# Kernel optimization log

Hardware: AMD Instinct MI355X
Metric: run time of the kernel (lower is better)

The kernel has to match this reference:

```python
import jax, jax.numpy as jnp
import numpy as np
import math

L, D, H, HD, F, G, V, P = 15, 512, 64, 8, 2048, 128, 7, 49
B, N = 4, 256


def setup_inputs() -> dict:
    key = jax.random.key(0)
    ks = jax.random.split(key, 24)
    nrm = lambda k, shape, s=0.02: (jax.random.normal(k, shape) * s).astype(jnp.float32)
    inp = {}
    inp["atom_types"] = jax.random.randint(ks[0], (B, N), 0, V)
    inp["coords"] = jax.random.normal(ks[1], (B, N, 3)) * 3.0
    inp["pair_types"] = jax.random.randint(ks[2], (B, N, N), 0, P)
    inp["mask"] = jnp.ones((B, N), dtype=bool)
    # embeddings / pair encoding params
    inp["atom_emb"] = nrm(ks[3], (V, D), 1.0).at[0].set(0.0)  # padding_idx=0
    inp["gaussian_mu"] = jax.random.normal(ks[4], (G,))
    inp["gaussian_sigma"] = jnp.ones((G,)) * 0.1
    inp["pair_a"] = jax.random.normal(ks[5], (P,)) * 0.01
    inp["pair_b"] = jax.random.normal(ks[6], (P,)) * 0.01
    inp["pl_w"] = nrm(ks[7], (G,))
    inp["pl_b"] = jnp.zeros(())
    # stacked per-layer params (leading dim L for lax.scan)
    inp["ln1_g"] = jnp.ones((L, D)); inp["ln1_b"] = jnp.zeros((L, D))
    inp["qkv_w"] = nrm(ks[8], (L, 3 * D, D)); inp["qkv_b"] = jnp.zeros((L, 3 * D))
    inp["pp_w"] = nrm(ks[9], (L, H), 0.1); inp["pp_b"] = jnp.zeros((L, H))
    inp["out_w"] = nrm(ks[10], (L, D, D)); inp["out_b"] = jnp.zeros((L, D))
    inp["ln2_g"] = jnp.ones((L, D)); inp["ln2_b"] = jnp.zeros((L, D))
    inp["ffn_w1"] = nrm(ks[11], (L, F, D)); inp["ffn_b1"] = jnp.zeros((L, F))
    inp["ffn_w2"] = nrm(ks[12], (L, D, F)); inp["ffn_b2"] = jnp.zeros((L, D))
    # SE3 head scalar affines (Linear(1,1) twice) and energy head
    inp["se3_uw"] = jnp.array(0.5); inp["se3_ub"] = jnp.array(0.01)
    inp["se3_ww"] = jnp.array(0.5); inp["se3_wb"] = jnp.array(0.01)
    inp["en_w"] = nrm(ks[13], (D,)); inp["en_b"] = jnp.zeros(())
    return inp


def _layernorm(x, g, b):
    m = x.mean(-1, keepdims=True)
    v = ((x - m) ** 2).mean(-1, keepdims=True)
    return (x - m) / jnp.sqrt(v + 1e-5) * g + b


def reference(atom_types, coords, pair_types, mask,
              atom_emb, gaussian_mu, gaussian_sigma, pair_a, pair_b, pl_w, pl_b,
              ln1_g, ln1_b, qkv_w, qkv_b, pp_w, pp_b, out_w, out_b,
              ln2_g, ln2_b, ffn_w1, ffn_b1, ffn_w2, ffn_b2,
              se3_uw, se3_ub, se3_ww, se3_wb, en_w, en_b):
    b_, n_ = atom_types.shape
    h = atom_emb[atom_types]  # [B,N,D]

    delta = coords[:, :, None, :] - coords[:, None, :, :]  # [B,N,N,3]
    d2 = (delta ** 2).sum(-1)
    dist = jnp.sqrt(jnp.maximum(d2, 1e-12))  # safe norm (grad-safe at 0)
    dist = jnp.where(mask[:, :, None], dist, 0.0)
    da = (pair_a[pair_types] * dist + pair_b[pair_types])[..., None]  # [B,N,N,1]
    gt = jnp.exp(-(da - gaussian_mu) ** 2) / (2.0 * gaussian_sigma ** 2)
    gt = gt / (gaussian_sigma * math.sqrt(2.0 * math.pi))
    gt = gt * mask[:, :, None, None]  # [B,N,N,G]
    pair_repr = gt @ pl_w + pl_b  # [B,N,N]
    pair_mask = mask[:, :, None] & mask[:, None, :]
    pair_repr = pair_repr * pair_mask

    scale = 1.0 / math.sqrt(HD)
    row_mask = mask[:, None, :, None]  # masks query rows, per original code

    def layer(hc, p):
        (l1g, l1b, qw, qb, ppw, ppb, ow, ob, l2g, l2b, w1, b1, w2, b2) = p
        x = _layernorm(hc, l1g, l1b)
        qkv = (x @ qw.T + qb).reshape(b_, n_, 3, H, HD)
        q, k, v = qkv[:, :, 0], qkv[:, :, 1], qkv[:, :, 2]
        scores = jnp.einsum('bnhd,bmhd->bhnm', q, k) * scale
        bias = pair_repr[..., None] * ppw + ppb  # [B,N,N,H]
        scores = scores + bias.transpose(0, 3, 1, 2)
        scores = jnp.where(row_mask, scores, -1e9)
        probs = jax.nn.softmax(scores, axis=-1)
        probs = jnp.where(jnp.isnan(probs), 0.0, probs)
        attn = jnp.einsum('bhnm,bmhd->bnhd', probs, v).reshape(b_, n_, D)
        hc = hc + attn @ ow.T + ob
        x2 = _layernorm(hc, l2g, l2b)
        ffn = jax.nn.gelu(x2 @ w1.T + b1, approximate=False) @ w2.T + b2
        return hc + ffn, None

    h, _ = jax.lax.scan(layer, h, (ln1_g, ln1_b, qkv_w, qkv_b, pp_w, pp_b,
                                   out_w, out_b, ln2_g, ln2_b,
                                   ffn_w1, ffn_b1, ffn_w2, ffn_b2))

    # --- SE3 equivariant head ---
    c = jax.nn.relu(pair_repr)[..., None]  # [B,N,N,1]
    c = c * se3_uw + se3_ub
    c = c * se3_ww + se3_wb
    c = c * mask[:, :, None, None]
    update = (delta * c).sum(axis=2)  # [B,N,3]
    num_valid = mask.sum(-1).astype(coords.dtype)[:, None, None] + 1e-6
    pred_coords = coords + update / num_valid

    cls = h[:, 0, :]
    pred_energy = cls @ en_w + en_b  # [B]
    return pred_coords, pred_energy


if __name__ == '__main__':
    out = reference(**setup_inputs())
    print(out[0].shape, out[1].shape)
```

## Files before the change

kernel.cpp:

```cpp
#include <hip/hip_runtime.h>
#include <hip/hip_bf16.h>
#include <math.h>

#define LAY 15
#define DIM 512
#define NH 64
#define HD 8
#define FF 2048
#define NG 128
#define BATCH 4
#define NTOK 256

typedef __attribute__((ext_vector_type(8))) short short8;
typedef __attribute__((ext_vector_type(4))) short short4v;
typedef __attribute__((ext_vector_type(8))) __bf16 bf16x8;
typedef __attribute__((ext_vector_type(4))) float f32x4;

__device__ inline short f2bs(float f) {
  __bf16 b = (__bf16)f;
  return __builtin_bit_cast(short, b);
}

__global__ __launch_bounds__(256) void embed_kernel(
    const int* __restrict__ types, const float* __restrict__ emb,
    float* __restrict__ h)
{
  int idx = blockIdx.x * 256 + threadIdx.x;
  int token = idx >> 9;
  int d = idx & 511;
  h[idx] = emb[types[token] * DIM + d];
}

__global__ __launch_bounds__(256) void cvt_kernel(
    const float* __restrict__ s, short* __restrict__ d, int n8)
{
  int i = blockIdx.x * 256 + threadIdx.x;
  if (i >= n8) return;
  const float4* sp = (const float4*)(s + (size_t)i * 8);
  float4 a = sp[0], b = sp[1];
  bf16x8 v;
  v[0] = (__bf16)a.x; v[1] = (__bf16)a.y; v[2] = (__bf16)a.z; v[3] = (__bf16)a.w;
  v[4] = (__bf16)b.x; v[5] = (__bf16)b.y; v[6] = (__bf16)b.z; v[7] = (__bf16)b.w;
  *(short8*)(d + (size_t)i * 8) = __builtin_bit_cast(short8, v);
}

__global__ __launch_bounds__(256) void pair_kernel(
    const int* __restrict__ pair_types, const float* __restrict__ coords,
    const float* __restrict__ mu, const float* __restrict__ sigma,
    const float* __restrict__ pa, const float* __restrict__ pb,
    const float* __restrict__ plw, const float* __restrict__ plb,
    float* __restrict__ pair_repr)
{
  __shared__ float smu[NG], sw[NG];
  int tid = threadIdx.x;
  if (tid < NG) {
    float sg = sigma[tid];
    smu[tid] = mu[tid];
    sw[tid] = plw[tid] / (2.0f * sg * sg * sg * 2.5066282746310002f);
  }
  __syncthreads();
  int idx = blockIdx.x * 256 + tid;
  int b = idx >> 16;
  int ij = idx & 65535;
  int i = ij >> 8, j = ij & 255;
  const float* ci = coords + (b * NTOK + i) * 3;
  const float* cj = coords + (b * NTOK + j) * 3;
  float dx = ci[0] - cj[0], dy = ci[1] - cj[1], dz = ci[2] - cj[2];
  float d2 = dx * dx + dy * dy + dz * dz;
  float dist = sqrtf(fmaxf(d2, 1e-12f));
  int pt = pair_types[idx];
  float da = pa[pt] * dist + pb[pt];
  float acc = 0.0f;
#pragma unroll 8
  for (int g = 0; g < NG; ++g) {
    float t = da - smu[g];
    acc += __expf(-t * t) * sw[g];
  }
  pair_repr[idx] = acc + plb[0];
}

__global__ __launch_bounds__(256) void pairT_kernel(
    const float* __restrict__ pr, float* __restrict__ prT)
{
  __shared__ float tile[32][33];
  int b = blockIdx.z;
  int i0 = blockIdx.y * 32, j0 = blockIdx.x * 32;
  int tx = threadIdx.x & 31, ty = threadIdx.x >> 5;
#pragma unroll
  for (int r = 0; r < 4; ++r)
    tile[ty + r * 8][tx] = pr[((size_t)(b * NTOK + i0 + ty + r * 8)) * NTOK + j0 + tx];
  __syncthreads();
#pragma unroll
  for (int r = 0; r < 4; ++r)
    prT[((size_t)(b * NTOK + j0 + ty + r * 8)) * NTOK + i0 + tx] = tile[tx][ty + r * 8];
}

__global__ __launch_bounds__(256) void coord_kernel(
    const float* __restrict__ coords, const float* __restrict__ pair_repr,
    const float* __restrict__ uw, const float* __restrict__ ub,
    const float* __restrict__ ww, const float* __restrict__ wb,
    float* __restrict__ out)
{
  int bi = blockIdx.x;
  int b = bi >> 8;
  int j = threadIdx.x;
  float pr = pair_repr[bi * 256 + j];
  float c = fmaxf(pr, 0.0f);
  c = c * uw[0] + ub[0];
  c = c * ww[0] + wb[0];
  const float* ci = coords + bi * 3;
  const float* cj = coords + (b * NTOK + j) * 3;
  float sx = (ci[0] - cj[0]) * c;
  float sy = (ci[1] - cj[1]) * c;
  float sz = (ci[2] - cj[2]) * c;
#pragma unroll
  for (int o = 32; o > 0; o >>= 1) {
    sx += __shfl_xor(sx, o);
    sy += __shfl_xor(sy, o);
    sz += __shfl_xor(sz, o);
  }
  __shared__ float sm[4][3];
  if ((j & 63) == 0) {
    sm[j >> 6][0] = sx; sm[j >> 6][1] = sy; sm[j >> 6][2] = sz;
  }
  __syncthreads();
  if (j < 3) {
    float u = sm[0][j] + sm[1][j] + sm[2][j] + sm[3][j];
    out[bi * 3 + j] = coords[bi * 3 + j] + u * (1.0f / (256.0f + 1e-6f));
  }
}

__global__ __launch_bounds__(256) void ln_kernel(
    const float* __restrict__ h, const float* __restrict__ g,
    const float* __restrict__ beta, short* __restrict__ x)
{
  int t = blockIdx.x;
  int tid = threadIdx.x;
  const float* hp = h + t * DIM;
  float v0 = hp[tid], v1 = hp[tid + 256];
  __shared__ float sm[4];
  float s = v0 + v1;
#pragma unroll
  for (int o = 32; o > 0; o >>= 1) s += __shfl_xor(s, o);
  if ((tid & 63) == 0) sm[tid >> 6] = s;
  __syncthreads();
  float mean = (sm[0] + sm[1] + sm[2] + sm[3]) * (1.0f / 512.0f);
  float d0 = v0 - mean, d1 = v1 - mean;
  float ss = d0 * d0 + d1 * d1;
#pragma unroll
  for (int o = 32; o > 0; o >>= 1) ss += __shfl_xor(ss, o);
  __syncthreads();
  if ((tid & 63) == 0) sm[tid >> 6] = ss;
  __syncthreads();
  float var = (sm[0] + sm[1] + sm[2] + sm[3]) * (1.0f / 512.0f);
  float rstd = rsqrtf(var + 1e-5f);
  x[t * DIM + tid] = f2bs(d0 * rstd * g[tid] + beta[tid]);
  x[t * DIM + tid + 256] = f2bs(d1 * rstd * g[tid + 256] + beta[tid + 256]);
}

template <int MODE>
__global__ __launch_bounds__(256) void mm2(
    const short* __restrict__ A, const short* __restrict__ W,
    const float* __restrict__ bias, float* __restrict__ Cf,
    short* __restrict__ Cb, int N, int K, int kparts)
{
  __shared__ short As[2][4096];
  __shared__ short Bs[2][4096];
  int tid = threadIdx.x;
  int lane = tid & 63, wv = tid >> 6;
  int wr = wv >> 1, wc = wv & 1;
  int fr = lane & 15, fq = lane >> 4;
  int m0 = blockIdx.y * 64, n0 = blockIdx.x * 64;
  int Ksub = K / kparts;
  int kbeg = blockIdx.z * Ksub, kend = kbeg + Ksub;

  int srow[2], scol[2];
#pragma unroll
  for (int r = 0; r < 2; ++r) {
    int id = r * 256 + tid;
    srow[r] = id >> 3;
    scol[r] = (id & 7) ^ (srow[r] & 7);
  }

  auto stage = [&](int p, int k0) {
#pragma unroll
    for (int r = 0; r < 2; ++r) {
      const short* ga = &A[(size_t)(m0 + srow[r]) * K + k0 + scol[r] * 8];
      __builtin_amdgcn_global_load_lds(
          (const __attribute__((address_space(1))) void*)ga,
          (__attribute__((address_space(3))) void*)&As[p][(r * 256 + wv * 64) * 8],
          16, 0, 0);
      const short* gw = &W[(size_t)(n0 + srow[r]) * K + k0 + scol[r] * 8];
      __builtin_amdgcn_global_load_lds(
          (const __attribute__((address_space(1))) void*)gw,
          (__attribute__((address_space(3))) void*)&Bs[p][(r * 256 + wv * 64) * 8],
          16, 0, 0);
    }
  };

  f32x4 acc[2][2];
#pragma unroll
  for (int i = 0; i < 2; ++i)
#pragma unroll
    for (int j = 0; j < 2; ++j) acc[i][j] = (f32x4){0.f, 0.f, 0.f, 0.f};

  int aslot[2][2], bslot[2][2];
#pragma unroll
  for (int s = 0; s < 2; ++s)
#pragma unroll
    for (int i = 0; i < 2; ++i) {
      int m = wr * 32 + i * 16 + fr;
      int c = s * 4 + fq;
      aslot[s][i] = m * 8 + (c ^ (m & 7));
      int n = wc * 32 + i * 16 + fr;
      bslot[s][i] = n * 8 + (c ^ (n & 7));
    }

  stage(0, kbeg);
  __syncthreads();
  int p = 0;
  for (int k0 = kbeg; k0 < kend; k0 += 64) {
    if (k0 + 64 < kend) stage(p ^ 1, k0 + 64);
    short8 af[2][2], bf_[2][2];
#pragma unroll
    for (int s = 0; s < 2; ++s)
#pragma unroll
      for (int i = 0; i < 2; ++i) {
        af[s][i] = *(const short8*)&As[p][aslot[s][i] * 8];
        bf_[s][i] = *(const short8*)&Bs[p][bslot[s][i] * 8];
      }
#pragma unroll
    for (int s = 0; s < 2; ++s)
#pragma unroll
      for (int i = 0; i < 2; ++i)
#pragma unroll
        for (int j = 0; j < 2; ++j)
          acc[i][j] = __builtin_amdgcn_mfma_f32_16x16x32_bf16(
              af[s][i], bf_[s][j], acc[i][j], 0, 0, 0);
    __syncthreads();
    p ^= 1;
  }

#pragma unroll
  for (int i = 0; i < 2; ++i) {
#pragma unroll
    for (int j = 0; j < 2; ++j) {
      int col = n0 + wc * 32 + j * 16 + fr;
      float bcol = bias[col];
#pragma unroll
      for (int rr = 0; rr < 4; ++rr) {
        int row = m0 + wr * 32 + i * 16 + fq * 4 + rr;
        size_t idx = (size_t)row * N + col;
        float v = acc[i][j][rr];
        if (MODE == 0) {
          Cf[idx] = v + bcol;
        } else if (MODE == 1) {
          if (blockIdx.z == 0) v += bcol;
          atomicAdd(&Cf[idx], v);
        } else if (MODE == 2) {
          v += bcol;
          Cb[idx] = f2bs(0.5f * v * (1.0f + erff(v * 0.70710678118654752f)));
        } else {
          Cb[idx] = f2bs(v + bcol);
        }
      }
    }
  }
}

__global__ __launch_bounds__(128) void attn_mfma(
    const short* __restrict__ qkv, const float* __restrict__ prT,
    const float* __restrict__ ppw, const float* __restrict__ ppb,
    short* __restrict__ attn)
{
  __shared__ alignas(16) short Kl[256 * 8];
  __shared__ alignas(16) short Ql[128 * 8];
  __shared__ alignas(16) short VT[8 * 264];
  __shared__ alignas(16) short P[2 * 16 * 264];
  __shared__ alignas(16) float linv[32];
  int h = blockIdx.x, b = blockIdx.y;
  int qbase = blockIdx.z * 128;
  int tid = threadIdx.x;

#pragma unroll
  for (int r0 = 0; r0 < 2; ++r0) {
    int r = tid + r0 * 128;
    short8 kv = *(const short8*)&qkv[(size_t)(b * NTOK + r) * 1536 + 512 + h * 8];
    *(short8*)&Kl[r * 8] = kv;
    short8 vv = *(const short8*)&qkv[(size_t)(b * NTOK + r) * 1536 + 1024 + h * 8];
#pragma unroll
    for (int d = 0; d < 8; ++d) VT[d * 264 + r] = vv[d];
  }
  {
    short8 qv = *(const short8*)&qkv[(size_t)(b * NTOK + qbase + tid) * 1536 + h * 8];
    *(short8*)&Ql[tid * 8] = qv;
  }
  __syncthreads();

  int lane = tid & 63, w = tid >> 6;
  int fr = lane & 15, quad = lane >> 4;
  float pw = ppw[h], pbb = ppb[h];
  const float scale = 0.35355339059327373f;
  short8 zero8 = {0, 0, 0, 0, 0, 0, 0, 0};

  short8 vfrag[8];
#pragma unroll
  for (int kc = 0; kc < 8; ++kc)
    vfrag[kc] = (fr < 8) ? *(const short8*)&VT[fr * 264 + kc * 32 + quad * 8]
                         : zero8;

  short* Pw = &P[w * 16 * 264];
  float* lw = &linv[w * 16];

  for (int qt = 0; qt < 4; ++qt) {
    int qloc = w * 64 + qt * 16;
    int qg = qbase + qloc + fr;
    const float* prp = &prT[(size_t)b * 65536 + qg];
    float prv[16][4];
#pragma unroll
    for (int t = 0; t < 16; ++t)
#pragma unroll
      for (int r = 0; r < 4; ++r)
        prv[t][r] = prp[(size_t)(t * 16 + quad * 4 + r) * NTOK];

    short8 qf = zero8;
    if (quad == 0) qf = *(const short8*)&Ql[(qloc + fr) * 8];
    f32x4 sacc[16];
#pragma unroll
    for (int t = 0; t < 16; ++t) {
      short8 kf = zero8;
      if (quad == 0) kf = *(const short8*)&Kl[(t * 16 + fr) * 8];
      sacc[t] = __builtin_amdgcn_mfma_f32_16x16x32_bf16(
          kf, qf, (f32x4){0.f, 0.f, 0.f, 0.f}, 0, 0, 0);
    }

    float l = 0.f;
#pragma unroll
    for (int t = 0; t < 16; ++t) {
      short4v pk;
#pragma unroll
      for (int r = 0; r < 4; ++r) {
        float s = sacc[t][r] * scale + prv[t][r] * pw + pbb;
        float p = __expf(s);
        l += p;
        pk[r] = f2bs(p);
      }
      *(short4v*)&Pw[fr * 264 + t * 16 + quad * 4] = pk;
    }
    l += __shfl_xor(l, 16);
    l += __shfl_xor(l, 32);
    if (lane < 16) lw[fr] = 1.0f / l;

    f32x4 oacc = (f32x4){0.f, 0.f, 0.f, 0.f};
#pragma unroll
    for (int kc = 0; kc < 8; ++kc) {
      short8 pf = *(const short8*)&Pw[fr * 264 + kc * 32 + quad * 8];
      oacc = __builtin_amdgcn_mfma_f32_16x16x32_bf16(pf, vfrag[kc], oacc, 0, 0, 0);
    }
    if (fr < 8) {
      f32x4 li = *(f32x4*)&lw[quad * 4];
#pragma unroll
      for (int r = 0; r < 4; ++r) {
        int q = qbase + qloc + quad * 4 + r;
        attn[(size_t)(b * NTOK + q) * DIM + h * 8 + fr] = f2bs(oacc[r] * li[r]);
      }
    }
  }
}

__global__ __launch_bounds__(256) void energy_kernel(
    const float* __restrict__ h, const float* __restrict__ enw,
    const float* __restrict__ enb, float* __restrict__ out)
{
  int b = blockIdx.x;
  int tid = threadIdx.x;
  const float* hp = h + b * NTOK * DIM;
  float s = hp[tid] * enw[tid] + hp[tid + 256] * enw[tid + 256];
  __shared__ float sm[4];
#pragma unroll
  for (int o = 32; o > 0; o >>= 1) s += __shfl_xor(s, o);
  if ((tid & 63) == 0) sm[tid >> 6] = s;
  __syncthreads();
  if (tid == 0) out[BATCH * NTOK * 3 + b] = sm[0] + sm[1] + sm[2] + sm[3] + enb[0];
}

extern "C" void kernel_launch(void* const* d_in, const int* in_sizes, int n_in,
                              void* d_out, int out_size, void* d_ws, size_t ws_size,
                              hipStream_t stream)
{
  const int*   atom_types = (const int*)d_in[0];
  const float* coords     = (const float*)d_in[1];
  const int*   pair_types = (const int*)d_in[2];
  const float* atom_emb = (const float*)d_in[4];
  const float* gmu  = (const float*)d_in[5];
  const float* gsig = (const float*)d_in[6];
  const float* pa   = (const float*)d_in[7];
  const float* pb   = (const float*)d_in[8];
  const float* plw  = (const float*)d_in[9];
  const float* plb  = (const float*)d_in[10];
  const float* ln1g = (const float*)d_in[11];
  const float* ln1b = (const float*)d_in[12];
  const float* qkvw = (const float*)d_in[13];
  const float* qkvb = (const float*)d_in[14];
  const float* ppw  = (const float*)d_in[15];
  const float* ppb  = (const float*)d_in[16];
  const float* outw = (const float*)d_in[17];
  const float* outb = (const float*)d_in[18];
  const float* ln2g = (const float*)d_in[19];
  const float* ln2b = (const float*)d_in[20];
  const float* w1   = (const float*)d_in[21];
  const float* b1   = (const float*)d_in[22];
  const float* w2   = (const float*)d_in[23];
  const float* b2   = (const float*)d_in[24];
  const float* uw   = (const float*)d_in[25];
  const float* ub   = (const float*)d_in[26];
  const float* sww  = (const float*)d_in[27];
  const float* swb  = (const float*)d_in[28];
  const float* enw  = (const float*)d_in[29];
  const float* enb  = (const float*)d_in[30];

  float* out = (float*)d_out;
  float* ws  = (float*)d_ws;
  float* pair_repr = ws;
  float* prT  = pair_repr + 262144;
  float* h    = prT + 262144;
  short* qkv_bf  = (short*)(h + 524288);
  short* x_bf    = qkv_bf + 1572864;
  short* attn_bf = x_bf + 524288;
  short* ffn1_bf = attn_bf + 524288;
  short* qkvw_bf = ffn1_bf + 2097152;
  short* outw_bf = qkvw_bf + 11796480;
  short* w1_bf   = outw_bf + 3932160;
  short* w2_bf   = w1_bf + 15728640;

  cvt_kernel<<<5760, 256, 0, stream>>>(qkvw, qkvw_bf, 1474560);
  cvt_kernel<<<1920, 256, 0, stream>>>(outw, outw_bf, 491520);
  cvt_kernel<<<7680, 256, 0, stream>>>(w1, w1_bf, 1966080);
  cvt_kernel<<<7680, 256, 0, stream>>>(w2, w2_bf, 1966080);

  embed_kernel<<<2048, 256, 0, stream>>>(atom_types, atom_emb, h);
  pair_kernel<<<1024, 256, 0, stream>>>(pair_types, coords, gmu, gsig, pa, pb,
                                        plw, plb, pair_repr);
  pairT_kernel<<<dim3(8, 8, 4), 256, 0, stream>>>(pair_repr, prT);
  coord_kernel<<<1024, 256, 0, stream>>>(coords, pair_repr, uw, ub, sww, swb, out);

  for (int l = 0; l < LAY; ++l) {
    ln_kernel<<<1024, 256, 0, stream>>>(h, ln1g + l * DIM, ln1b + l * DIM, x_bf);
    mm2<3><<<dim3(24, 16, 1), 256, 0, stream>>>(
        x_bf, qkvw_bf + (size_t)l * 1536 * DIM, qkvb + l * 1536, nullptr, qkv_bf,
        1536, DIM, 1);
    attn_mfma<<<dim3(NH, BATCH, 2), 128, 0, stream>>>(
        qkv_bf, prT, ppw + l * NH, ppb + l * NH, attn_bf);
    mm2<1><<<dim3(8, 16, 4), 256, 0, stream>>>(
        attn_bf, outw_bf + (size_t)l * DIM * DIM, outb + l * DIM, h, nullptr,
        DIM, DIM, 4);
    ln_kernel<<<1024, 256, 0, stream>>>(h, ln2g + l * DIM, ln2b + l * DIM, x_bf);
    mm2<2><<<dim3(32, 16, 1), 256, 0, stream>>>(
        x_bf, w1_bf + (size_t)l * FF * DIM, b1 + l * FF, nullptr, ffn1_bf,
        FF, DIM, 1);
    mm2<1><<<dim3(8, 16, 4), 256, 0, stream>>>(
        ffn1_bf, w2_bf + (size_t)l * DIM * FF, b2 + l * DIM, h, nullptr,
        DIM, FF, 4);
  }
  energy_kernel<<<BATCH, 256, 0, stream>>>(h, enw, enb, out);
}
```

Before: 1.270 ms.

## Fuse LayerNorm into QKV and FFN1 GEMM A-tile staging; merge weight conversions

Removes the standalone LayerNorm kernels. Each GEMM block now computes per-row mean and rstd for its 64 rows from the fp32 hidden state, then normalizes and converts the A tiles to bf16 while staging them into LDS. This saves two launches per layer and the bf16 round trip through global memory. In exchange, every column block recomputes the row statistics and re-reads fp32 activations (24 or 32 times redundantly). The variance now uses the E[x²]−μ² form. The four weight-conversion launches are also merged into one kernel.

```diff
diff --git a/kernel.cpp b/kernel.cpp
--- a/kernel.cpp
+++ b/kernel.cpp
@@ -31,17 +31,23 @@
   h[idx] = emb[types[token] * DIM + d];
 }
 
-__global__ __launch_bounds__(256) void cvt_kernel(
-    const float* __restrict__ s, short* __restrict__ d, int n8)
+__global__ __launch_bounds__(256) void cvt_all_kernel(
+    const float* __restrict__ qkvw, const float* __restrict__ outw,
+    const float* __restrict__ w1, const float* __restrict__ w2,
+    short* __restrict__ dst)
 {
   int i = blockIdx.x * 256 + threadIdx.x;
-  if (i >= n8) return;
-  const float4* sp = (const float4*)(s + (size_t)i * 8);
+  const float* src;
+  if (i < 1474560)      src = qkvw + (size_t)i * 8;
+  else if (i < 1966080) src = outw + ((size_t)i - 1474560) * 8;
+  else if (i < 3932160) src = w1 + ((size_t)i - 1966080) * 8;
+  else                  src = w2 + ((size_t)i - 3932160) * 8;
+  const float4* sp = (const float4*)src;
   float4 a = sp[0], b = sp[1];
   bf16x8 v;
   v[0] = (__bf16)a.x; v[1] = (__bf16)a.y; v[2] = (__bf16)a.z; v[3] = (__bf16)a.w;
   v[4] = (__bf16)b.x; v[5] = (__bf16)b.y; v[6] = (__bf16)b.z; v[7] = (__bf16)b.w;
-  *(short8*)(d + (size_t)i * 8) = __builtin_bit_cast(short8, v);
+  *(short8*)(dst + (size_t)i * 8) = __builtin_bit_cast(short8, v);
 }
 
 __global__ __launch_bounds__(256) void pair_kernel(
@@ -130,32 +136,152 @@
   }
 }
 
-__global__ __launch_bounds__(256) void ln_kernel(
-    const float* __restrict__ h, const float* __restrict__ g,
-    const float* __restrict__ beta, short* __restrict__ x)
-{
-  int t = blockIdx.x;
+template <int MODE>
+__global__ __launch_bounds__(256) void mmln(
+    const float* __restrict__ H, const float* __restrict__ g,
+    const float* __restrict__ beta, const short* __restrict__ W,
+    const float* __restrict__ bias, short* __restrict__ Cb, int N)
+{
+  __shared__ short As[2][4096];
+  __shared__ short Bs[2][4096];
+  __shared__ float mean_s[64], rstd_s[64];
   int tid = threadIdx.x;
-  const float* hp = h + t * DIM;
-  float v0 = hp[tid], v1 = hp[tid + 256];
-  __shared__ float sm[4];
-  float s = v0 + v1;
-#pragma unroll
-  for (int o = 32; o > 0; o >>= 1) s += __shfl_xor(s, o);
-  if ((tid & 63) == 0) sm[tid >> 6] = s;
-  __syncthreads();
-  float mean = (sm[0] + sm[1] + sm[2] + sm[3]) * (1.0f / 512.0f);
-  float d0 = v0 - mean, d1 = v1 - mean;
-  float ss = d0 * d0 + d1 * d1;
-#pragma unroll
-  for (int o = 32; o > 0; o >>= 1) ss += __shfl_xor(ss, o);
-  __syncthreads();
-  if ((tid & 63) == 0) sm[tid >> 6] = ss;
-  __syncthreads();
-  float var = (sm[0] + sm[1] + sm[2] + sm[3]) * (1.0f / 512.0f);
-  float rstd = rsqrtf(var + 1e-5f);
-  x[t * DIM + tid] = f2bs(d0 * rstd * g[tid] + beta[tid]);
-  x[t * DIM + tid + 256] = f2bs(d1 * rstd * g[tid + 256] + beta[tid + 256]);
+  int lane = tid & 63, wv = tid >> 6;
+  int wr = wv >> 1, wc = wv & 1;
+  int fr = lane & 15, fq = lane >> 4;
+  int m0 = blockIdx.y * 64, n0 = blockIdx.x * 64;
+
+  for (int rr = 0; rr < 16; ++rr) {
+    int row = wv * 16 + rr;
+    const float* hp = &H[(size_t)(m0 + row) * DIM + lane * 8];
+    float4 x0 = *(const float4*)hp;
+    float4 x1 = *(const float4*)(hp + 4);
+    float s1 = x0.x + x0.y + x0.z + x0.w + x1.x + x1.y + x1.z + x1.w;
+    float s2 = x0.x * x0.x + x0.y * x0.y + x0.z * x0.z + x0.w * x0.w +
+               x1.x * x1.x + x1.y * x1.y + x1.z * x1.z + x1.w * x1.w;
+#pragma unroll
+    for (int o = 32; o > 0; o >>= 1) {
+      s1 += __shfl_xor(s1, o);
+      s2 += __shfl_xor(s2, o);
+    }
+    if (lane == 0) {
+      float mu = s1 * (1.0f / 512.0f);
+      float var = s2 * (1.0f / 512.0f) - mu * mu;
+      mean_s[row] = mu;
+      rstd_s[row] = rsqrtf(var + 1e-5f);
+    }
+  }
+  __syncthreads();
+
+  int srow[2], scol[2];
+#pragma unroll
+  for (int r = 0; r < 2; ++r) {
+    int id = r * 256 + tid;
+    srow[r] = id >> 3;
+    scol[r] = (id & 7) ^ (srow[r] & 7);
+  }
+
+  auto stageB = [&](int p, int k0) {
+#pragma unroll
+    for (int r = 0; r < 2; ++r) {
+      const short* gw = &W[(size_t)(n0 + srow[r]) * DIM + k0 + scol[r] * 8];
+      __builtin_amdgcn_global_load_lds(
+          (const __attribute__((address_space(1))) void*)gw,
+          (__attribute__((address_space(3))) void*)&Bs[p][(r * 256 + wv * 64) * 8],
+          16, 0, 0);
+    }
+  };
+  auto stageA = [&](int p, int k0) {
+#pragma unroll
+    for (int r = 0; r < 2; ++r) {
+      int row = srow[r];
+      int k = k0 + scol[r] * 8;
+      const float* hp = &H[(size_t)(m0 + row) * DIM + k];
+      float4 a0 = *(const float4*)hp;
+      float4 a1 = *(const float4*)(hp + 4);
+      float4 g0 = *(const float4*)&g[k];
+      float4 g1 = *(const float4*)&g[k + 4];
+      float4 b0 = *(const float4*)&beta[k];
+      float4 b1 = *(const float4*)&beta[k + 4];
+      float mu = mean_s[row], rs = rstd_s[row];
+      bf16x8 v;
+      v[0] = (__bf16)((a0.x - mu) * rs * g0.x + b0.x);
+      v[1] = (__bf16)((a0.y - mu) * rs * g0.y + b0.y);
+      v[2] = (__bf16)((a0.z - mu) * rs * g0.z + b0.z);
+      v[3] = (__bf16)((a0.w - mu) * rs * g0.w + b0.w);
+      v[4] = (__bf16)((a1.x - mu) * rs * g1.x + b1.x);
+      v[5] = (__bf16)((a1.y - mu) * rs * g1.y + b1.y);
+      v[6] = (__bf16)((a1.z - mu) * rs * g1.z + b1.z);
+      v[7] = (__bf16)((a1.w - mu) * rs * g1.w + b1.w);
+      *(short8*)&As[p][(r * 256 + tid) * 8] = __builtin_bit_cast(short8, v);
+    }
+  };
+
+  f32x4 acc[2][2];
+#pragma unroll
+  for (int i = 0; i < 2; ++i)
+#pragma unroll
+    for (int j = 0; j < 2; ++j) acc[i][j] = (f32x4){0.f, 0.f, 0.f, 0.f};
+
+  int aslot[2][2], bslot[2][2];
+#pragma unroll
+  for (int s = 0; s < 2; ++s)
+#pragma unroll
+    for (int i = 0; i < 2; ++i) {
+      int m = wr * 32 + i * 16 + fr;
+      int c = s * 4 + fq;
+      aslot[s][i] = m * 8 + (c ^ (m & 7));
+      int n = wc * 32 + i * 16 + fr;
+      bslot[s][i] = n * 8 + (c ^ (n & 7));
+    }
+
+  stageB(0, 0);
+  stageA(0, 0);
+  __syncthreads();
+  int p = 0;
+  for (int k0 = 0; k0 < DIM; k0 += 64) {
+    if (k0 + 64 < DIM) {
+      stageB(p ^ 1, k0 + 64);
+      stageA(p ^ 1, k0 + 64);
+    }
+    short8 af[2][2], bf_[2][2];
+#pragma unroll
+    for (int s = 0; s < 2; ++s)
+#pragma unroll
+      for (int i = 0; i < 2; ++i) {
+        af[s][i] = *(const short8*)&As[p][aslot[s][i] * 8];
+        bf_[s][i] = *(const short8*)&Bs[p][bslot[s][i] * 8];
+      }
+#pragma unroll
+    for (int s = 0; s < 2; ++s)
+#pragma unroll
+      for (int i = 0; i < 2; ++i)
+#pragma unroll
+        for (int j = 0; j < 2; ++j)
+          acc[i][j] = __builtin_amdgcn_mfma_f32_16x16x32_bf16(
+              af[s][i], bf_[s][j], acc[i][j], 0, 0, 0);
+    __syncthreads();
+    p ^= 1;
+  }
+
+#pragma unroll
+  for (int i = 0; i < 2; ++i) {
+#pragma unroll
+    for (int j = 0; j < 2; ++j) {
+      int col = n0 + wc * 32 + j * 16 + fr;
+      float bcol = bias[col];
+#pragma unroll
+      for (int rr = 0; rr < 4; ++rr) {
+        int row = m0 + wr * 32 + i * 16 + fq * 4 + rr;
+        size_t idx = (size_t)row * N + col;
+        float v = acc[i][j][rr] + bcol;
+        if (MODE == 2)
+          Cb[idx] = f2bs(0.5f * v * (1.0f + erff(v * 0.70710678118654752f)));
+        else
+          Cb[idx] = f2bs(v);
+      }
+    }
+  }
 }
 
 template <int MODE>
@@ -252,16 +378,11 @@
         int row = m0 + wr * 32 + i * 16 + fq * 4 + rr;
         size_t idx = (size_t)row * N + col;
         float v = acc[i][j][rr];
-        if (MODE == 0) {
-          Cf[idx] = v + bcol;
-        } else if (MODE == 1) {
+        if (MODE == 1) {
           if (blockIdx.z == 0) v += bcol;
           atomicAdd(&Cf[idx], v);
-        } else if (MODE == 2) {
-          v += bcol;
-          Cb[idx] = f2bs(0.5f * v * (1.0f + erff(v * 0.70710678118654752f)));
         } else {
-          Cb[idx] = f2bs(v + bcol);
+          Cf[idx] = v + bcol;
         }
       }
     }
@@ -425,18 +546,14 @@
   float* prT  = pair_repr + 262144;
   float* h    = prT + 262144;
   short* qkv_bf  = (short*)(h + 524288);
-  short* x_bf    = qkv_bf + 1572864;
-  short* attn_bf = x_bf + 524288;
+  short* attn_bf = qkv_bf + 1572864;
   short* ffn1_bf = attn_bf + 524288;
   short* qkvw_bf = ffn1_bf + 2097152;
   short* outw_bf = qkvw_bf + 11796480;
   short* w1_bf   = outw_bf + 3932160;
   short* w2_bf   = w1_bf + 15728640;
 
-  cvt_kernel<<<5760, 256, 0, stream>>>(qkvw, qkvw_bf, 1474560);
-  cvt_kernel<<<1920, 256, 0, stream>>>(outw, outw_bf, 491520);
-  cvt_kernel<<<7680, 256, 0, stream>>>(w1, w1_bf, 1966080);
-  cvt_kernel<<<7680, 256, 0, stream>>>(w2, w2_bf, 1966080);
+  cvt_all_kernel<<<23040, 256, 0, stream>>>(qkvw, outw, w1, w2, qkvw_bf);
 
   embed_kernel<<<2048, 256, 0, stream>>>(atom_types, atom_emb, h);
   pair_kernel<<<1024, 256, 0, stream>>>(pair_types, coords, gmu, gsig, pa, pb,
@@ -445,19 +562,17 @@
   coord_kernel<<<1024, 256, 0, stream>>>(coords, pair_repr, uw, ub, sww, swb, out);
 
   for (int l = 0; l < LAY; ++l) {
-    ln_kernel<<<1024, 256, 0, stream>>>(h, ln1g + l * DIM, ln1b + l * DIM, x_bf);
-    mm2<3><<<dim3(24, 16, 1), 256, 0, stream>>>(
-        x_bf, qkvw_bf + (size_t)l * 1536 * DIM, qkvb + l * 1536, nullptr, qkv_bf,
-        1536, DIM, 1);
+    mmln<3><<<dim3(24, 16, 1), 256, 0, stream>>>(
+        h, ln1g + l * DIM, ln1b + l * DIM,
+        qkvw_bf + (size_t)l * 1536 * DIM, qkvb + l * 1536, qkv_bf, 1536);
     attn_mfma<<<dim3(NH, BATCH, 2), 128, 0, stream>>>(
         qkv_bf, prT, ppw + l * NH, ppb + l * NH, attn_bf);
     mm2<1><<<dim3(8, 16, 4), 256, 0, stream>>>(
         attn_bf, outw_bf + (size_t)l * DIM * DIM, outb + l * DIM, h, nullptr,
         DIM, DIM, 4);
-    ln_kernel<<<1024, 256, 0, stream>>>(h, ln2g + l * DIM, ln2b + l * DIM, x_bf);
-    mm2<2><<<dim3(32, 16, 1), 256, 0, stream>>>(
-        x_bf, w1_bf + (size_t)l * FF * DIM, b1 + l * FF, nullptr, ffn1_bf,
-        FF, DIM, 1);
+    mmln<2><<<dim3(32, 16, 1), 256, 0, stream>>>(
+        h, ln2g + l * DIM, ln2b + l * DIM,
+        w1_bf + (size_t)l * FF * DIM, b1 + l * FF, ffn1_bf, FF);
     mm2<1><<<dim3(8, 16, 4), 256, 0, stream>>>(
         ffn1_bf, w2_bf + (size_t)l * DIM * FF, b2 + l * DIM, h, nullptr,
         DIM, FF, 4);
```

New measurement: 1.551 ms. 22.2% more time.

## Shrink GEMM tiles to 32x64 with two waves and merge weight conversions

Applied to the files above, without the earlier changes.

The GEMM kernel now uses 128-thread blocks computing 32x64 output tiles, which doubles the grid along M, and the out-projection split-K drops from 4 to 2 parts. This raises block count and occupancy on the many CUs, at the cost of less operand reuse per block and more global traffic for the weight tiles. The four weight-conversion launches are merged into one kernel that relies on the bf16 buffers being contiguous.

```diff
diff --git a/kernel.cpp b/kernel.cpp
--- a/kernel.cpp
+++ b/kernel.cpp
@@ -31,17 +31,23 @@
   h[idx] = emb[types[token] * DIM + d];
 }
 
-__global__ __launch_bounds__(256) void cvt_kernel(
-    const float* __restrict__ s, short* __restrict__ d, int n8)
+__global__ __launch_bounds__(256) void cvt_all_kernel(
+    const float* __restrict__ qkvw, const float* __restrict__ outw,
+    const float* __restrict__ w1, const float* __restrict__ w2,
+    short* __restrict__ dst)
 {
   int i = blockIdx.x * 256 + threadIdx.x;
-  if (i >= n8) return;
-  const float4* sp = (const float4*)(s + (size_t)i * 8);
+  const float* src;
+  if (i < 1474560)      src = qkvw + (size_t)i * 8;
+  else if (i < 1966080) src = outw + ((size_t)i - 1474560) * 8;
+  else if (i < 3932160) src = w1 + ((size_t)i - 1966080) * 8;
+  else                  src = w2 + ((size_t)i - 3932160) * 8;
+  const float4* sp = (const float4*)src;
   float4 a = sp[0], b = sp[1];
   bf16x8 v;
   v[0] = (__bf16)a.x; v[1] = (__bf16)a.y; v[2] = (__bf16)a.z; v[3] = (__bf16)a.w;
   v[4] = (__bf16)b.x; v[5] = (__bf16)b.y; v[6] = (__bf16)b.z; v[7] = (__bf16)b.w;
-  *(short8*)(d + (size_t)i * 8) = __builtin_bit_cast(short8, v);
+  *(short8*)(dst + (size_t)i * 8) = __builtin_bit_cast(short8, v);
 }
 
 __global__ __launch_bounds__(256) void pair_kernel(
@@ -159,41 +165,49 @@
 }
 
 template <int MODE>
-__global__ __launch_bounds__(256) void mm2(
+__global__ __launch_bounds__(128) void mm3(
     const short* __restrict__ A, const short* __restrict__ W,
     const float* __restrict__ bias, float* __restrict__ Cf,
     short* __restrict__ Cb, int N, int K, int kparts)
 {
-  __shared__ short As[2][4096];
+  __shared__ short As[2][2048];
   __shared__ short Bs[2][4096];
   int tid = threadIdx.x;
   int lane = tid & 63, wv = tid >> 6;
-  int wr = wv >> 1, wc = wv & 1;
   int fr = lane & 15, fq = lane >> 4;
-  int m0 = blockIdx.y * 64, n0 = blockIdx.x * 64;
+  int m0 = blockIdx.y * 32, n0 = blockIdx.x * 64;
   int Ksub = K / kparts;
   int kbeg = blockIdx.z * Ksub, kend = kbeg + Ksub;
 
-  int srow[2], scol[2];
+  int arow[2], acol[2], brow[4], bcol[4];
 #pragma unroll
   for (int r = 0; r < 2; ++r) {
-    int id = r * 256 + tid;
-    srow[r] = id >> 3;
-    scol[r] = (id & 7) ^ (srow[r] & 7);
+    int id = r * 128 + tid;
+    arow[r] = id >> 3;
+    acol[r] = (id & 7) ^ (arow[r] & 7);
+  }
+#pragma unroll
+  for (int r = 0; r < 4; ++r) {
+    int id = r * 128 + tid;
+    brow[r] = id >> 3;
+    bcol[r] = (id & 7) ^ (brow[r] & 7);
   }
 
   auto stage = [&](int p, int k0) {
 #pragma unroll
     for (int r = 0; r < 2; ++r) {
-      const short* ga = &A[(size_t)(m0 + srow[r]) * K + k0 + scol[r] * 8];
+      const short* ga = &A[(size_t)(m0 + arow[r]) * K + k0 + acol[r] * 8];
       __builtin_amdgcn_global_load_lds(
           (const __attribute__((address_space(1))) void*)ga,
-          (__attribute__((address_space(3))) void*)&As[p][(r * 256 + wv * 64) * 8],
+          (__attribute__((address_space(3))) void*)&As[p][(r * 128 + wv * 64) * 8],
           16, 0, 0);
-      const short* gw = &W[(size_t)(n0 + srow[r]) * K + k0 + scol[r] * 8];
+    }
+#pragma unroll
+    for (int r = 0; r < 4; ++r) {
+      const short* gw = &W[(size_t)(n0 + brow[r]) * K + k0 + bcol[r] * 8];
       __builtin_amdgcn_global_load_lds(
           (const __attribute__((address_space(1))) void*)gw,
-          (__attribute__((address_space(3))) void*)&Bs[p][(r * 256 + wv * 64) * 8],
+          (__attribute__((address_space(3))) void*)&Bs[p][(r * 128 + wv * 64) * 8],
           16, 0, 0);
     }
   };
@@ -209,10 +223,10 @@
   for (int s = 0; s < 2; ++s)
 #pragma unroll
     for (int i = 0; i < 2; ++i) {
-      int m = wr * 32 + i * 16 + fr;
+      int m = i * 16 + fr;
       int c = s * 4 + fq;
       aslot[s][i] = m * 8 + (c ^ (m & 7));
-      int n = wc * 32 + i * 16 + fr;
+      int n = wv * 32 + i * 16 + fr;
       bslot[s][i] = n * 8 + (c ^ (n & 7));
     }
 
@@ -245,16 +259,14 @@
   for (int i = 0; i < 2; ++i) {
 #pragma unroll
     for (int j = 0; j < 2; ++j) {
-      int col = n0 + wc * 32 + j * 16 + fr;
+      int col = n0 + wv * 32 + j * 16 + fr;
       float bcol = bias[col];
 #pragma unroll
       for (int rr = 0; rr < 4; ++rr) {
-        int row = m0 + wr * 32 + i * 16 + fq * 4 + rr;
+        int row = m0 + i * 16 + fq * 4 + rr;
         size_t idx = (size_t)row * N + col;
         float v = acc[i][j][rr];
-        if (MODE == 0) {
-          Cf[idx] = v + bcol;
-        } else if (MODE == 1) {
+        if (MODE == 1) {
           if (blockIdx.z == 0) v += bcol;
           atomicAdd(&Cf[idx], v);
         } else if (MODE == 2) {
@@ -433,10 +445,7 @@
   short* w1_bf   = outw_bf + 3932160;
   short* w2_bf   = w1_bf + 15728640;
 
-  cvt_kernel<<<5760, 256, 0, stream>>>(qkvw, qkvw_bf, 1474560);
-  cvt_kernel<<<1920, 256, 0, stream>>>(outw, outw_bf, 491520);
-  cvt_kernel<<<7680, 256, 0, stream>>>(w1, w1_bf, 1966080);
-  cvt_kernel<<<7680, 256, 0, stream>>>(w2, w2_bf, 1966080);
+  cvt_all_kernel<<<23040, 256, 0, stream>>>(qkvw, outw, w1, w2, qkvw_bf);
 
   embed_kernel<<<2048, 256, 0, stream>>>(atom_types, atom_emb, h);
   pair_kernel<<<1024, 256, 0, stream>>>(pair_types, coords, gmu, gsig, pa, pb,
@@ -446,19 +455,19 @@
 
   for (int l = 0; l < LAY; ++l) {
     ln_kernel<<<1024, 256, 0, stream>>>(h, ln1g + l * DIM, ln1b + l * DIM, x_bf);
-    mm2<3><<<dim3(24, 16, 1), 256, 0, stream>>>(
+    mm3<3><<<dim3(24, 32, 1), 128, 0, stream>>>(
         x_bf, qkvw_bf + (size_t)l * 1536 * DIM, qkvb + l * 1536, nullptr, qkv_bf,
         1536, DIM, 1);
     attn_mfma<<<dim3(NH, BATCH, 2), 128, 0, stream>>>(
         qkv_bf, prT, ppw + l * NH, ppb + l * NH, attn_bf);
-    mm2<1><<<dim3(8, 16, 4), 256, 0, stream>>>(
+    mm3<1><<<dim3(8, 32, 2), 128, 0, stream>>>(
         attn_bf, outw_bf + (size_t)l * DIM * DIM, outb + l * DIM, h, nullptr,
-        DIM, DIM, 4);
+        DIM, DIM, 2);
     ln_kernel<<<1024, 256, 0, stream>>>(h, ln2g + l * DIM, ln2b + l * DIM, x_bf);
-    mm2<2><<<dim3(32, 16, 1), 256, 0, stream>>>(
+    mm3<2><<<dim3(32, 32, 1), 128, 0, stream>>>(
         x_bf, w1_bf + (size_t)l * FF * DIM, b1 + l * FF, nullptr, ffn1_bf,
         FF, DIM, 1);
-    mm2<1><<<dim3(8, 16, 4), 256, 0, stream>>>(
+    mm3<1><<<dim3(8, 32, 4), 128, 0, stream>>>(
         ffn1_bf, w2_bf + (size_t)l * DIM * FF, b2 + l * DIM, h, nullptr,
         DIM, FF, 4);
   }
```

New measurement: 1.241 ms. 2.3% less time.
